# Performance work log

Measured on AMD Instinct MI355X. Metric: run time of the kernel, lower is better.

The kernel has to match this reference:

```python
import jax, jax.numpy as jnp
import numpy as np

EPS = 1e-8  # matches torch F.cosine_similarity eps


def setup_inputs() -> dict:
    key = jax.random.key(0)
    k1, k2, k3 = jax.random.split(key, 3)
    S, B, H = 16, 512, 2048
    OGLogits = jax.random.normal(k1, (B, H), dtype=jnp.float32)
    enhancedSamplesLogits = jax.random.normal(k2, (S, B, H), dtype=jnp.float32)
    W = jax.random.normal(k3, (H, H), dtype=jnp.float32) * (1.0 / np.sqrt(H))
    b = jnp.zeros((H,), dtype=jnp.float32)
    return {"OGLogits": OGLogits, "enhancedSamplesLogits": enhancedSamplesLogits, "W": W, "b": b}


def reference(OGLogits, enhancedSamplesLogits, W, b):
    # Original torch code builds the full (S*B, B) cosine-similarity matrix and
    # keeps only the diagonal via an eye mask; mathematically that equals the
    # per-pair cosine similarity cos(enhanced[s,b], OG[b]), computed directly here.
    e_norm = jnp.linalg.norm(enhancedSamplesLogits, axis=-1)          # (S, B)
    o_norm = jnp.linalg.norm(OGLogits, axis=-1)                       # (B,)
    dots = jnp.einsum('sbh,bh->sb', enhancedSamplesLogits, OGLogits)  # (S, B)
    sims = dots / jnp.maximum(e_norm * o_norm[None, :], EPS)          # (S, B)
    weighted = enhancedSamplesLogits * sims[..., None]                # (S, B, H)
    weightedRep = weighted.mean(axis=0)                               # (B, H)
    return weightedRep @ W.T + b                                      # (B, H)
```

## Files before the change

kernel.cpp:

```cpp
#include <hip/hip_runtime.h>

#define S_DIM 16
#define B_DIM 512
#define H_DIM 2048
#define EPS 1e-8f

typedef short bf16x8 __attribute__((ext_vector_type(8)));
typedef float f32x16 __attribute__((ext_vector_type(16)));

__device__ __forceinline__ unsigned short f2bf(float f) {
    union { float f; unsigned int u; } v; v.f = f;
    unsigned int u = v.u;
    unsigned int r = (u + 0x7fffu + ((u >> 16) & 1u)) >> 16;
    return (unsigned short)r;
}

__device__ __forceinline__ float dot4(const float4& a, const float4& b) {
    return a.x*b.x + a.y*b.y + a.z*b.z + a.w*b.w;
}

__global__ __launch_bounds__(256) void sims_kernel(
    const float* __restrict__ OG, const float* __restrict__ E,
    const float* __restrict__ W, float* __restrict__ sims,
    unsigned short* __restrict__ Wb) {
    const int bid = blockIdx.x;
    if (bid < (S_DIM * B_DIM / 4)) {
        const int lane = threadIdx.x & 63;
        const int r = bid * 4 + (threadIdx.x >> 6);
        const int b = r & (B_DIM - 1);
        const float4* e4  = (const float4*)E  + (size_t)r * (H_DIM / 4);
        const float4* og4 = (const float4*)OG + (size_t)b * (H_DIM / 4);
        float d = 0.f, n = 0.f, o = 0.f;
        #pragma unroll
        for (int i = 0; i < 8; ++i) {
            float4 e = e4[i * 64 + lane];
            float4 g = og4[i * 64 + lane];
            d += dot4(e, g); n += dot4(e, e); o += dot4(g, g);
        }
        #pragma unroll
        for (int m = 32; m >= 1; m >>= 1) {
            d += __shfl_xor(d, m, 64);
            n += __shfl_xor(n, m, 64);
            o += __shfl_xor(o, m, 64);
        }
        if (lane == 0) sims[r] = d / fmaxf(sqrtf(n) * sqrtf(o), EPS);
    } else {
        const int wb = bid - (S_DIM * B_DIM / 4);
        const int t = threadIdx.x;
        const float4* w4 = (const float4*)W;
        ushort4* wb4 = (ushort4*)Wb;
        #pragma unroll
        for (int j = 0; j < 8; ++j) {
            const size_t idx = (size_t)wb * 2048 + j * 256 + t;
            float4 v = w4[idx];
            ushort4 c;
            c.x = f2bf(v.x); c.y = f2bf(v.y); c.z = f2bf(v.z); c.w = f2bf(v.w);
            wb4[idx] = c;
        }
    }
}

__global__ __launch_bounds__(512) void wmean_kernel(
    const float* __restrict__ E, const float* __restrict__ sims,
    unsigned short* __restrict__ wrep) {
    const int b = blockIdx.x;
    const int t = threadIdx.x;
    __shared__ float sl[S_DIM];
    const float4* e4 = (const float4*)E;
    float4 ev[S_DIM];
    #pragma unroll
    for (int s = 0; s < S_DIM; ++s)
        ev[s] = e4[((size_t)s * B_DIM + b) * (H_DIM / 4) + t];
    if (t < S_DIM) sl[t] = sims[t * B_DIM + b];
    __syncthreads();
    float x = 0.f, y = 0.f, z = 0.f, w = 0.f;
    #pragma unroll
    for (int s = 0; s < S_DIM; ++s) {
        const float sm = sl[s];
        x += sm * ev[s].x; y += sm * ev[s].y;
        z += sm * ev[s].z; w += sm * ev[s].w;
    }
    const float sc = 1.f / (float)S_DIM;
    ushort4 ob;
    ob.x = f2bf(x * sc); ob.y = f2bf(y * sc);
    ob.z = f2bf(z * sc); ob.w = f2bf(w * sc);
    ((ushort4*)wrep)[(size_t)b * (H_DIM / 4) + t] = ob;
}

__global__ __launch_bounds__(256) void gemm_kernel(
    const unsigned short* __restrict__ A, const unsigned short* __restrict__ Wb,
    const float* __restrict__ bias, float* __restrict__ out) {
    const int n0 = blockIdx.x * 64;
    const int m0 = blockIdx.y * 64;

    __shared__ unsigned short As[2][64][72];
    __shared__ unsigned short Bs[2][64][72];

    const int t = threadIdx.x;
    const int lane = t & 63;
    const int wave = t >> 6;
    const int wm = (wave & 1) * 32;
    const int wn = (wave >> 1) * 32;

    const int lr = t >> 2, lq = t & 3;
    const unsigned short* ap = A  + (size_t)(m0 + lr) * H_DIM + lq * 16;
    const unsigned short* bp = Wb + (size_t)(n0 + lr) * H_DIM + lq * 16;

    f32x16 acc = {0.f,0.f,0.f,0.f,0.f,0.f,0.f,0.f,
                  0.f,0.f,0.f,0.f,0.f,0.f,0.f,0.f};

    const int row = lane & 31;
    const int hi = lane >> 5;

    uint4 a0 = *(const uint4*)(ap);
    uint4 a1 = *(const uint4*)(ap + 8);
    uint4 b0 = *(const uint4*)(bp);
    uint4 b1 = *(const uint4*)(bp + 8);
    *(uint4*)&As[0][lr][lq * 16]     = a0;
    *(uint4*)&As[0][lr][lq * 16 + 8] = a1;
    *(uint4*)&Bs[0][lr][lq * 16]     = b0;
    *(uint4*)&Bs[0][lr][lq * 16 + 8] = b1;
    __syncthreads();

    for (int ki = 0; ki < 32; ++ki) {
        const int cur = ki & 1, nxt = cur ^ 1;
        if (ki + 1 < 32) {
            a0 = *(const uint4*)(ap + (ki + 1) * 64);
            a1 = *(const uint4*)(ap + (ki + 1) * 64 + 8);
            b0 = *(const uint4*)(bp + (ki + 1) * 64);
            b1 = *(const uint4*)(bp + (ki + 1) * 64 + 8);
        }
        #pragma unroll
        for (int ks = 0; ks < 4; ++ks) {
            bf16x8 af  = *(const bf16x8*)&As[cur][wm + row][ks * 16 + hi * 8];
            bf16x8 bfr = *(const bf16x8*)&Bs[cur][wn + row][ks * 16 + hi * 8];
            acc = __builtin_amdgcn_mfma_f32_32x32x16_bf16(af, bfr, acc, 0, 0, 0);
        }
        if (ki + 1 < 32) {
            *(uint4*)&As[nxt][lr][lq * 16]     = a0;
            *(uint4*)&As[nxt][lr][lq * 16 + 8] = a1;
            *(uint4*)&Bs[nxt][lr][lq * 16]     = b0;
            *(uint4*)&Bs[nxt][lr][lq * 16 + 8] = b1;
        }
        __syncthreads();
    }

    const int col = lane & 31;
    const float bias0 = bias[n0 + wn + col];
    #pragma unroll
    for (int r = 0; r < 16; ++r) {
        const int mr = (r & 3) + 8 * (r >> 2) + 4 * hi;
        out[(size_t)(m0 + wm + mr) * H_DIM + n0 + wn + col] = acc[r] + bias0;
    }
}

extern "C" void kernel_launch(void* const* d_in, const int* in_sizes, int n_in,
                              void* d_out, int out_size, void* d_ws, size_t ws_size,
                              hipStream_t stream) {
    const float* OG   = (const float*)d_in[0];
    const float* E    = (const float*)d_in[1];
    const float* W    = (const float*)d_in[2];
    const float* bias = (const float*)d_in[3];
    float* out = (float*)d_out;

    unsigned short* wrep = (unsigned short*)d_ws;
    unsigned short* Wb   = wrep + (size_t)B_DIM * H_DIM;
    float* sims          = (float*)(Wb + (size_t)H_DIM * H_DIM);

    sims_kernel<<<(S_DIM * B_DIM / 4) + 512, 256, 0, stream>>>(OG, E, W, sims, Wb);
    wmean_kernel<<<B_DIM, 512, 0, stream>>>(E, sims, wrep);
    gemm_kernel<<<dim3(H_DIM / 64, B_DIM / 64), 256, 0, stream>>>(wrep, Wb, bias, out);
}
```

Measured before the change: 141.3 us.

## Fuse cosine-sim and weighted-mean into one kernel, split GEMM accumulators

Merges the similarity kernel and the weighted-mean kernel into one block-per-batch kernel. Each wave handles two samples, computes their cosine similarities in registers and reduces the weighted rows through shared memory, so E is read once instead of twice and the sims buffer disappears. The W-to-bf16 conversion moves into the same kernel. In the GEMM, the MFMA chain is split into two independent accumulators to shorten the dependency chain. The cost is 64KB of LDS and many registers per block in the fused kernel, which limits occupancy with only 512 blocks.

```diff
diff --git a/kernel.cpp b/kernel.cpp
--- a/kernel.cpp
+++ b/kernel.cpp
@@ -19,72 +19,84 @@
     return a.x*b.x + a.y*b.y + a.z*b.z + a.w*b.w;
 }
 
-__global__ __launch_bounds__(256) void sims_kernel(
+__global__ __launch_bounds__(512) void fused_kernel(
     const float* __restrict__ OG, const float* __restrict__ E,
-    const float* __restrict__ W, float* __restrict__ sims,
+    const float* __restrict__ W, unsigned short* __restrict__ wrep,
     unsigned short* __restrict__ Wb) {
-    const int bid = blockIdx.x;
-    if (bid < (S_DIM * B_DIM / 4)) {
-        const int lane = threadIdx.x & 63;
-        const int r = bid * 4 + (threadIdx.x >> 6);
-        const int b = r & (B_DIM - 1);
-        const float4* e4  = (const float4*)E  + (size_t)r * (H_DIM / 4);
-        const float4* og4 = (const float4*)OG + (size_t)b * (H_DIM / 4);
-        float d = 0.f, n = 0.f, o = 0.f;
-        #pragma unroll
-        for (int i = 0; i < 8; ++i) {
-            float4 e = e4[i * 64 + lane];
-            float4 g = og4[i * 64 + lane];
-            d += dot4(e, g); n += dot4(e, e); o += dot4(g, g);
-        }
-        #pragma unroll
-        for (int m = 32; m >= 1; m >>= 1) {
-            d += __shfl_xor(d, m, 64);
-            n += __shfl_xor(n, m, 64);
-            o += __shfl_xor(o, m, 64);
-        }
-        if (lane == 0) sims[r] = d / fmaxf(sqrtf(n) * sqrtf(o), EPS);
-    } else {
-        const int wb = bid - (S_DIM * B_DIM / 4);
-        const int t = threadIdx.x;
-        const float4* w4 = (const float4*)W;
-        ushort4* wb4 = (ushort4*)Wb;
-        #pragma unroll
-        for (int j = 0; j < 8; ++j) {
-            const size_t idx = (size_t)wb * 2048 + j * 256 + t;
-            float4 v = w4[idx];
-            ushort4 c;
-            c.x = f2bf(v.x); c.y = f2bf(v.y); c.z = f2bf(v.z); c.w = f2bf(v.w);
-            wb4[idx] = c;
-        }
-    }
-}
-
-__global__ __launch_bounds__(512) void wmean_kernel(
-    const float* __restrict__ E, const float* __restrict__ sims,
-    unsigned short* __restrict__ wrep) {
     const int b = blockIdx.x;
     const int t = threadIdx.x;
-    __shared__ float sl[S_DIM];
-    const float4* e4 = (const float4*)E;
-    float4 ev[S_DIM];
+    const int lane = t & 63;
+    const int wave = t >> 6;
+
+    __shared__ float4 buf[8][512];
+
+    const float4* e4a = (const float4*)(E + ((size_t)wave * B_DIM + b) * H_DIM);
+    const float4* e4b = (const float4*)(E + ((size_t)(wave + 8) * B_DIM + b) * H_DIM);
+    const float4* og4 = (const float4*)(OG + (size_t)b * H_DIM);
+
+    float4 ea[8], eb[8], og[8];
     #pragma unroll
-    for (int s = 0; s < S_DIM; ++s)
-        ev[s] = e4[((size_t)s * B_DIM + b) * (H_DIM / 4) + t];
-    if (t < S_DIM) sl[t] = sims[t * B_DIM + b];
+    for (int i = 0; i < 8; ++i) {
+        const int c = (i + wave) & 7;
+        ea[i] = e4a[c * 64 + lane];
+        eb[i] = e4b[c * 64 + lane];
+        og[i] = og4[c * 64 + lane];
+    }
+
+    float da = 0.f, na = 0.f, db = 0.f, nb = 0.f, o2 = 0.f;
+    #pragma unroll
+    for (int i = 0; i < 8; ++i) {
+        da += dot4(ea[i], og[i]);
+        na += dot4(ea[i], ea[i]);
+        db += dot4(eb[i], og[i]);
+        nb += dot4(eb[i], eb[i]);
+        o2 += dot4(og[i], og[i]);
+    }
+    #pragma unroll
+    for (int m = 32; m >= 1; m >>= 1) {
+        da += __shfl_xor(da, m, 64);
+        na += __shfl_xor(na, m, 64);
+        db += __shfl_xor(db, m, 64);
+        nb += __shfl_xor(nb, m, 64);
+        o2 += __shfl_xor(o2, m, 64);
+    }
+    const float onorm = sqrtf(o2);
+    const float sima = da / fmaxf(sqrtf(na) * onorm, EPS);
+    const float simb = db / fmaxf(sqrtf(nb) * onorm, EPS);
+
+    #pragma unroll
+    for (int i = 0; i < 8; ++i) {
+        const int c = (i + wave) & 7;
+        float4 v;
+        v.x = ea[i].x * sima + eb[i].x * simb;
+        v.y = ea[i].y * sima + eb[i].y * simb;
+        v.z = ea[i].z * sima + eb[i].z * simb;
+        v.w = ea[i].w * sima + eb[i].w * simb;
+        buf[wave][c * 64 + lane] = v;
+    }
     __syncthreads();
-    float x = 0.f, y = 0.f, z = 0.f, w = 0.f;
+
+    float4 s = buf[0][t];
     #pragma unroll
-    for (int s = 0; s < S_DIM; ++s) {
-        const float sm = sl[s];
-        x += sm * ev[s].x; y += sm * ev[s].y;
-        z += sm * ev[s].z; w += sm * ev[s].w;
+    for (int w = 1; w < 8; ++w) {
+        float4 v = buf[w][t];
+        s.x += v.x; s.y += v.y; s.z += v.z; s.w += v.w;
     }
     const float sc = 1.f / (float)S_DIM;
     ushort4 ob;
-    ob.x = f2bf(x * sc); ob.y = f2bf(y * sc);
-    ob.z = f2bf(z * sc); ob.w = f2bf(w * sc);
+    ob.x = f2bf(s.x * sc); ob.y = f2bf(s.y * sc);
+    ob.z = f2bf(s.z * sc); ob.w = f2bf(s.w * sc);
     ((ushort4*)wrep)[(size_t)b * (H_DIM / 4) + t] = ob;
+
+    const float4* w4 = (const float4*)W;
+    #pragma unroll
+    for (int j = 0; j < 4; ++j) {
+        const size_t idx = (size_t)b * 2048 + j * 512 + t;
+        float4 v = w4[idx];
+        ushort4 c;
+        c.x = f2bf(v.x); c.y = f2bf(v.y); c.z = f2bf(v.z); c.w = f2bf(v.w);
+        ((ushort4*)Wb)[idx] = c;
+    }
 }
 
 __global__ __launch_bounds__(256) void gemm_kernel(
@@ -106,8 +118,10 @@
     const unsigned short* ap = A  + (size_t)(m0 + lr) * H_DIM + lq * 16;
     const unsigned short* bp = Wb + (size_t)(n0 + lr) * H_DIM + lq * 16;
 
-    f32x16 acc = {0.f,0.f,0.f,0.f,0.f,0.f,0.f,0.f,
-                  0.f,0.f,0.f,0.f,0.f,0.f,0.f,0.f};
+    f32x16 acc0 = {0.f,0.f,0.f,0.f,0.f,0.f,0.f,0.f,
+                   0.f,0.f,0.f,0.f,0.f,0.f,0.f,0.f};
+    f32x16 acc1 = {0.f,0.f,0.f,0.f,0.f,0.f,0.f,0.f,
+                   0.f,0.f,0.f,0.f,0.f,0.f,0.f,0.f};
 
     const int row = lane & 31;
     const int hi = lane >> 5;
@@ -131,10 +145,13 @@
             b1 = *(const uint4*)(bp + (ki + 1) * 64 + 8);
         }
         #pragma unroll
-        for (int ks = 0; ks < 4; ++ks) {
-            bf16x8 af  = *(const bf16x8*)&As[cur][wm + row][ks * 16 + hi * 8];
-            bf16x8 bfr = *(const bf16x8*)&Bs[cur][wn + row][ks * 16 + hi * 8];
-            acc = __builtin_amdgcn_mfma_f32_32x32x16_bf16(af, bfr, acc, 0, 0, 0);
+        for (int ks = 0; ks < 2; ++ks) {
+            bf16x8 afA = *(const bf16x8*)&As[cur][wm + row][ks * 16 + hi * 8];
+            bf16x8 bfA = *(const bf16x8*)&Bs[cur][wn + row][ks * 16 + hi * 8];
+            acc0 = __builtin_amdgcn_mfma_f32_32x32x16_bf16(afA, bfA, acc0, 0, 0, 0);
+            bf16x8 afB = *(const bf16x8*)&As[cur][wm + row][(ks + 2) * 16 + hi * 8];
+            bf16x8 bfB = *(const bf16x8*)&Bs[cur][wn + row][(ks + 2) * 16 + hi * 8];
+            acc1 = __builtin_amdgcn_mfma_f32_32x32x16_bf16(afB, bfB, acc1, 0, 0, 0);
         }
         if (ki + 1 < 32) {
             *(uint4*)&As[nxt][lr][lq * 16]     = a0;
@@ -150,7 +167,7 @@
     #pragma unroll
     for (int r = 0; r < 16; ++r) {
         const int mr = (r & 3) + 8 * (r >> 2) + 4 * hi;
-        out[(size_t)(m0 + wm + mr) * H_DIM + n0 + wn + col] = acc[r] + bias0;
+        out[(size_t)(m0 + wm + mr) * H_DIM + n0 + wn + col] = acc0[r] + acc1[r] + bias0;
     }
 }
 
@@ -165,9 +182,7 @@
 
     unsigned short* wrep = (unsigned short*)d_ws;
     unsigned short* Wb   = wrep + (size_t)B_DIM * H_DIM;
-    float* sims          = (float*)(Wb + (size_t)H_DIM * H_DIM);
 
-    sims_kernel<<<(S_DIM * B_DIM / 4) + 512, 256, 0, stream>>>(OG, E, W, sims, Wb);
-    wmean_kernel<<<B_DIM, 512, 0, stream>>>(E, sims, wrep);
+    fused_kernel<<<B_DIM, 512, 0, stream>>>(OG, E, W, wrep, Wb);
     gemm_kernel<<<dim3(H_DIM / 64, B_DIM / 64), 256, 0, stream>>>(wrep, Wb, bias, out);
 }
```

Result: faster. 126.1 us (-10.7%).
